# Kernel tuning notes

Measured on AMD Instinct MI355X. Metric: run time of the kernel, lower is better.

## Reference

```python
import jax, jax.numpy as jnp
import numpy as np

N_NODES = 20000
N_EDGES = 320000
IN_F = 168
HID = 256


def gcn_conv(x, W, b, src, dst, ew, n_nodes):
    """PyG GCNConv: symmetric normalization with self-loops (fill 1.0).
    out = D^-1/2 (A + I) D^-1/2 X W^T + b, aggregated at dst (source_to_target).
    """
    xw = x @ W.T  # [N, F_out]
    # degree at target nodes, including self-loop weight 1.0
    deg = jax.ops.segment_sum(ew, dst, num_segments=n_nodes) + 1.0
    dinv = jnp.where(deg > 0, jax.lax.rsqrt(deg), 0.0)
    norm = dinv[src] * ew * dinv[dst]  # [E]
    agg = jax.ops.segment_sum(norm[:, None] * xw[src], dst, num_segments=n_nodes)
    # self-loop contribution: norm_ii = dinv[i]^2
    out = agg + (dinv * dinv)[:, None] * xw
    return out + b


def setup_inputs() -> dict:
    key = jax.random.key(0)
    k = jax.random.split(key, 8)
    x = jax.random.normal(k[0], (N_NODES, IN_F), dtype=jnp.float32)
    edge_index = jax.random.randint(k[1], (2, N_EDGES), 0, N_NODES, dtype=jnp.int64)
    edge_weight = jax.random.uniform(k[2], (N_EDGES,), dtype=jnp.float32)
    # GCN layer weights (PyG Linear: y = x W^T), plus per-layer bias
    s1 = 1.0 / np.sqrt(IN_F)
    s2 = 1.0 / np.sqrt(HID)
    W1 = jax.random.uniform(k[3], (HID, IN_F), minval=-s1, maxval=s1, dtype=jnp.float32)
    b1 = jnp.zeros((HID,), dtype=jnp.float32)
    W2 = jax.random.uniform(k[4], (HID, HID), minval=-s2, maxval=s2, dtype=jnp.float32)
    b2 = jnp.zeros((HID,), dtype=jnp.float32)
    return {"x": x, "edge_index": edge_index, "edge_weight": edge_weight,
            "W1": W1, "b1": b1, "W2": W2, "b2": b2}


def reference(x, edge_index, edge_weight, W1, b1, W2, b2):
    src, dst = edge_index[0], edge_index[1]
    h = gcn_conv(x, W1, b1, src, dst, edge_weight, N_NODES)
    h = jax.nn.relu(h)
    h = gcn_conv(h, W2, b2, src, dst, edge_weight, N_NODES)
    h = jax.nn.relu(h)
    return h
```

## Files before the change

kernel.cpp:

```cpp
#include <hip/hip_runtime.h>

#define N_NODES 20000
#define N_EDGES 320000
#define IN_F    168
#define HID     256
#define K1P     192
#define XS      192
#define NF4     42

typedef __attribute__((ext_vector_type(8))) short bf16x8;
typedef __attribute__((ext_vector_type(4))) float f32x4;

__device__ __forceinline__ short f2bf(float f) {
    union { float f; unsigned u; } v; v.f = f;
    unsigned r = v.u + 0x7FFFu + ((v.u >> 16) & 1u);
    return (short)(r >> 16);
}
__device__ __forceinline__ float bf2f(short s) {
    union { unsigned u; float f; } v; v.u = ((unsigned)(unsigned short)s) << 16;
    return v.f;
}


__global__ void prep_all(const float* __restrict__ x, short* __restrict__ xb,
                         const float* __restrict__ W1, const float* __restrict__ W2,
                         short* __restrict__ w1b, short* __restrict__ w2b,
                         const int* __restrict__ ei, const float* __restrict__ ew,
                         float* __restrict__ deg, int* __restrict__ counts) {
    int b = blockIdx.x;
    int k = threadIdx.x;
    if (b < N_NODES) {
        if (k >= XS) return;
        float v = (k < IN_F) ? x[(size_t)b * IN_F + k] : 0.f;
        xb[(size_t)b * XS + k] = f2bf(v);
        return;
    }
    b -= N_NODES;
    if (b < 256) {
        if (k >= K1P) return;
        float v = (k < IN_F) ? W1[(size_t)b * IN_F + k] : 0.f;
        w1b[(size_t)b * K1P + k] = f2bf(v);
        return;
    }
    if (b < 512) {
        int r = b - 256;
        w2b[(size_t)r * HID + k] = f2bf(W2[(size_t)r * HID + k]);
        return;
    }
    int e = (b - 512) * 256 + k;
    if (e < N_EDGES) {
        int d = ei[N_EDGES + e];
        atomicAdd(&deg[d], ew[e]);
        atomicAdd(&counts[d], 1);
    }
}


__global__ __launch_bounds__(1024) void scan_part(const int* __restrict__ counts,
                                                  int* __restrict__ offs,
                                                  int* __restrict__ bsum,
                                                  float* __restrict__ deg, int n) {
    int tid  = threadIdx.x;
    int lane = tid & 63;
    int wv   = tid >> 6;
    int i = blockIdx.x * 1024 + tid;
    if (i < n) deg[i] = rsqrtf(deg[i] + 1.0f);
    __shared__ int wsum[16];
    int v = (i < n) ? counts[i] : 0;
    int incl = v;
    #pragma unroll
    for (int d = 1; d < 64; d <<= 1) {
        int t = __shfl_up(incl, d);
        if (lane >= d) incl += t;
    }
    if (lane == 63) wsum[wv] = incl;
    __syncthreads();
    if (wv == 0) {
        int w = (lane < 16) ? wsum[lane] : 0;
        int winc = w;
        #pragma unroll
        for (int d = 1; d < 16; d <<= 1) {
            int t = __shfl_up(winc, d);
            if (lane >= d) winc += t;
        }
        if (lane < 16) wsum[lane] = winc - w;
    }
    __syncthreads();
    if (i < n) offs[i] = wsum[wv] + incl - v;
    if (tid == 1023) bsum[blockIdx.x] = wsum[15] + incl;
}

__global__ __launch_bounds__(1024) void scan_add(const int* __restrict__ bsum,
                                                 int* __restrict__ offs, int n) {
    int i = blockIdx.x * 1024 + threadIdx.x;
    int add = 0;
    for (int b = 0; b < (int)blockIdx.x; ++b) add += bsum[b];
    if (i < n) offs[i] += add;
    if (i == n) offs[n] = add + bsum[blockIdx.x];
}

__global__ void scatter_edges(const int* __restrict__ ei, const float* __restrict__ ew,
                              const float* __restrict__ dinv, const int* __restrict__ offs,
                              int* __restrict__ cursor, int2* __restrict__ er) {
    int e = blockIdx.x * blockDim.x + threadIdx.x;
    if (e >= N_EDGES) return;
    int s = ei[e];
    int d = ei[N_EDGES + e];
    int pos = offs[d] + atomicAdd(&cursor[d], 1);
    float nm = dinv[s] * ew[e] * dinv[d];
    er[pos] = make_int2(s, __float_as_int(nm));
}


__global__ __launch_bounds__(256) void agg_x(const short* __restrict__ xb,
                                             const float* __restrict__ dinv,
                                             const int* __restrict__ offs,
                                             const int2* __restrict__ er,
                                             short* __restrict__ ax) {
    int wave = threadIdx.x >> 6;
    int lane = threadIdx.x & 63;
    int n = blockIdx.x * 4 + wave;
    bool act = lane < NF4;
    int lo4 = act ? lane * 4 : 0;
    float di = dinv[n];
    float sw = di * di;
    short4 sv = *(const short4*)(xb + (size_t)n * XS + lo4);
    float a0 = sw * bf2f(sv.x), a1 = sw * bf2f(sv.y);
    float a2 = sw * bf2f(sv.z), a3 = sw * bf2f(sv.w);

    int p0 = offs[n], p1 = offs[n + 1];
    int p = p0;
    for (; p + 8 <= p1; p += 8) {
        int2 e[8]; short4 r[8];
        #pragma unroll
        for (int j = 0; j < 8; ++j) e[j] = er[p + j];
        #pragma unroll
        for (int j = 0; j < 8; ++j) r[j] = *(const short4*)(xb + (size_t)e[j].x * XS + lo4);
        #pragma unroll
        for (int j = 0; j < 8; ++j) {
            float w = __int_as_float(e[j].y);
            a0 += w * bf2f(r[j].x); a1 += w * bf2f(r[j].y);
            a2 += w * bf2f(r[j].z); a3 += w * bf2f(r[j].w);
        }
    }
    for (; p + 4 <= p1; p += 4) {
        int2 e[4]; short4 r[4];
        #pragma unroll
        for (int j = 0; j < 4; ++j) e[j] = er[p + j];
        #pragma unroll
        for (int j = 0; j < 4; ++j) r[j] = *(const short4*)(xb + (size_t)e[j].x * XS + lo4);
        #pragma unroll
        for (int j = 0; j < 4; ++j) {
            float w = __int_as_float(e[j].y);
            a0 += w * bf2f(r[j].x); a1 += w * bf2f(r[j].y);
            a2 += w * bf2f(r[j].z); a3 += w * bf2f(r[j].w);
        }
    }
    for (; p < p1; ++p) {
        int2 e0 = er[p];
        float w0 = __int_as_float(e0.y);
        short4 r0 = *(const short4*)(xb + (size_t)e0.x * XS + lo4);
        a0 += w0 * bf2f(r0.x); a1 += w0 * bf2f(r0.y);
        a2 += w0 * bf2f(r0.z); a3 += w0 * bf2f(r0.w);
    }

    size_t base = (size_t)n * K1P + lane * 4;
    if (act) {
        *(short4*)&ax[base] = make_short4(f2bf(a0), f2bf(a1), f2bf(a2), f2bf(a3));
    } else if (lane < 48) {
        *(short4*)&ax[base] = make_short4(0, 0, 0, 0);
    }
}

__global__ __launch_bounds__(256) void agg_h(const short* __restrict__ h1h,
                                             const float* __restrict__ dinv,
                                             const int* __restrict__ offs,
                                             const int2* __restrict__ er,
                                             short* __restrict__ ah) {
    int wave = threadIdx.x >> 6;
    int lane = threadIdx.x & 63;
    int n = blockIdx.x * 4 + wave;
    int lo4 = lane * 4;
    float di = dinv[n];
    float sw = di * di;
    short4 sv = *(const short4*)(h1h + (size_t)n * HID + lo4);
    float a0 = sw * bf2f(sv.x), a1 = sw * bf2f(sv.y);
    float a2 = sw * bf2f(sv.z), a3 = sw * bf2f(sv.w);

    int p0 = offs[n], p1 = offs[n + 1];
    int p = p0;
    for (; p + 8 <= p1; p += 8) {
        int2 e[8]; short4 r[8];
        #pragma unroll
        for (int j = 0; j < 8; ++j) e[j] = er[p + j];
        #pragma unroll
        for (int j = 0; j < 8; ++j) r[j] = *(const short4*)(h1h + (size_t)e[j].x * HID + lo4);
        #pragma unroll
        for (int j = 0; j < 8; ++j) {
            float w = __int_as_float(e[j].y);
            a0 += w * bf2f(r[j].x); a1 += w * bf2f(r[j].y);
            a2 += w * bf2f(r[j].z); a3 += w * bf2f(r[j].w);
        }
    }
    for (; p + 4 <= p1; p += 4) {
        int2 e[4]; short4 r[4];
        #pragma unroll
        for (int j = 0; j < 4; ++j) e[j] = er[p + j];
        #pragma unroll
        for (int j = 0; j < 4; ++j) r[j] = *(const short4*)(h1h + (size_t)e[j].x * HID + lo4);
        #pragma unroll
        for (int j = 0; j < 4; ++j) {
            float w = __int_as_float(e[j].y);
            a0 += w * bf2f(r[j].x); a1 += w * bf2f(r[j].y);
            a2 += w * bf2f(r[j].z); a3 += w * bf2f(r[j].w);
        }
    }
    for (; p < p1; ++p) {
        int2 e0 = er[p];
        float w0 = __int_as_float(e0.y);
        short4 r0 = *(const short4*)(h1h + (size_t)e0.x * HID + lo4);
        a0 += w0 * bf2f(r0.x); a1 += w0 * bf2f(r0.y);
        a2 += w0 * bf2f(r0.z); a3 += w0 * bf2f(r0.w);
    }

    size_t base = (size_t)n * HID + lo4;
    *(short4*)&ah[base] = make_short4(f2bf(a0), f2bf(a1), f2bf(a2), f2bf(a3));
}


#define LDS_STRIDE 72

__global__ __launch_bounds__(256) void gemm_bf(const short* __restrict__ Ah,
                                               const short* __restrict__ Wh,
                                               const float* __restrict__ bias,
                                               float* __restrict__ Cf,
                                               short* __restrict__ Cbf,
                                               int M, int Ks, int nsteps, int mode) {
    __shared__ short sAh[64 * LDS_STRIDE];
    __shared__ short sWh[64 * LDS_STRIDE];

    const int idx   = blockIdx.x;
    const int group = idx >> 5;
    const int xcd   = idx & 7;
    const int slot  = (idx >> 3) & 3;
    const int mt    = group * 8 + xcd;
    const int mtiles = (M + 63) >> 6;
    if (mt >= mtiles) return;
    const int bm = mt * 64;
    const int bn = slot * 64;

    const int tid  = threadIdx.x;
    const int lane = tid & 63;
    const int wv   = tid >> 6;
    const int l16  = lane & 15;
    const int quad = lane >> 4;
    const int wm   = (wv & 1) * 32;
    const int wn   = (wv >> 1) * 32;

    const int srow = tid >> 2;
    const int sseg = (tid & 3) * 16;
    int arow = bm + srow; if (arow >= M) arow = M - 1;
    const short* gAh = Ah + (size_t)arow * Ks;
    const short* gWh = Wh + (size_t)(bn + srow) * Ks;
    const int lds_off = srow * LDS_STRIDE + sseg;

    f32x4 acc00 = {0,0,0,0}, acc01 = {0,0,0,0}, acc10 = {0,0,0,0}, acc11 = {0,0,0,0};

    int4 pah0 = *(const int4*)(gAh + sseg), pah1 = *(const int4*)(gAh + sseg + 8);
    int4 pwh0 = *(const int4*)(gWh + sseg), pwh1 = *(const int4*)(gWh + sseg + 8);

    for (int ks = 0; ks < nsteps; ++ks) {
        *(int4*)&sAh[lds_off] = pah0; *(int4*)&sAh[lds_off + 8] = pah1;
        *(int4*)&sWh[lds_off] = pwh0; *(int4*)&sWh[lds_off + 8] = pwh1;
        __syncthreads();
        if (ks + 1 < nsteps) {
            int o = (ks + 1) * 64 + sseg;
            pah0 = *(const int4*)(gAh + o); pah1 = *(const int4*)(gAh + o + 8);
            pwh0 = *(const int4*)(gWh + o); pwh1 = *(const int4*)(gWh + o + 8);
        }
        #pragma unroll
        for (int o = 0; o < 2; ++o) {
            const int a0 = (wm + l16) * LDS_STRIDE + o * 32 + quad * 8;
            const int a1 = a0 + 16 * LDS_STRIDE;
            const int w0 = (wn + l16) * LDS_STRIDE + o * 32 + quad * 8;
            const int w1 = w0 + 16 * LDS_STRIDE;
            bf16x8 ah0 = *(const bf16x8*)&sAh[a0];
            bf16x8 ah1 = *(const bf16x8*)&sAh[a1];
            bf16x8 wh0 = *(const bf16x8*)&sWh[w0];
            bf16x8 wh1 = *(const bf16x8*)&sWh[w1];
            acc00 = __builtin_amdgcn_mfma_f32_16x16x32_bf16(ah0, wh0, acc00, 0, 0, 0);
            acc01 = __builtin_amdgcn_mfma_f32_16x16x32_bf16(ah0, wh1, acc01, 0, 0, 0);
            acc10 = __builtin_amdgcn_mfma_f32_16x16x32_bf16(ah1, wh0, acc10, 0, 0, 0);
            acc11 = __builtin_amdgcn_mfma_f32_16x16x32_bf16(ah1, wh1, acc11, 0, 0, 0);
        }
        __syncthreads();
    }

    const int colb = bn + wn + l16;
    const int rowb = bm + wm + quad * 4;
    const float b0 = bias[colb];
    const float b1 = bias[colb + 16];
    #pragma unroll
    for (int r = 0; r < 4; ++r) {
        int row = rowb + r;
        if (row < M) {
            float v0 = acc00[r] + b0; v0 = v0 > 0.f ? v0 : 0.f;
            float v1 = acc01[r] + b1; v1 = v1 > 0.f ? v1 : 0.f;
            if (mode == 0) {
                Cbf[(size_t)row * HID + colb]      = f2bf(v0);
                Cbf[(size_t)row * HID + colb + 16] = f2bf(v1);
            } else {
                Cf[(size_t)row * HID + colb]      = v0;
                Cf[(size_t)row * HID + colb + 16] = v1;
            }
        }
        int row2 = row + 16;
        if (row2 < M) {
            float v0 = acc10[r] + b0; v0 = v0 > 0.f ? v0 : 0.f;
            float v1 = acc11[r] + b1; v1 = v1 > 0.f ? v1 : 0.f;
            if (mode == 0) {
                Cbf[(size_t)row2 * HID + colb]      = f2bf(v0);
                Cbf[(size_t)row2 * HID + colb + 16] = f2bf(v1);
            } else {
                Cf[(size_t)row2 * HID + colb]      = v0;
                Cf[(size_t)row2 * HID + colb + 16] = v1;
            }
        }
    }
}


extern "C" void kernel_launch(void* const* d_in, const int* in_sizes, int n_in,
                              void* d_out, int out_size, void* d_ws, size_t ws_size,
                              hipStream_t stream) {
    const float* x  = (const float*)d_in[0];
    const int*   ei = (const int*)d_in[1];
    const float* ew = (const float*)d_in[2];
    const float* W1 = (const float*)d_in[3];
    const float* b1 = (const float*)d_in[4];
    const float* W2 = (const float*)d_in[5];
    const float* b2 = (const float*)d_in[6];
    float* out = (float*)d_out;

    char* ws = (char*)d_ws;
    float* deg      = (float*)(ws);
    int*   counts   = (int*)(ws + 80000);
    int*   cursor   = (int*)(ws + 160000);
    int*   offs     = (int*)(ws + 240000);
    int*   bsum     = (int*)(ws + 320016);
    int2*  er       = (int2*)(ws + 320144);
    short* ax       = (short*)(ws + 2880144);
    short* ah       = (short*)(ws + 2880144);
    short* h1h      = (short*)(ws + 23360144);
    short* w1b      = (short*)(ws + 33600144);
    short* w2b      = (short*)(ws + 33698448);
    short* xb       = (short*)(ws + 34058896);

    hipMemsetAsync(d_ws, 0, 240000, stream);

    const int TB = 256;
    prep_all<<<N_NODES + 512 + (N_EDGES + 255) / 256, 256, 0, stream>>>(
        x, xb, W1, W2, w1b, w2b, ei, ew, deg, counts);
    scan_part<<<20, 1024, 0, stream>>>(counts, offs, bsum, deg, N_NODES);
    scan_add<<<20, 1024, 0, stream>>>(bsum, offs, N_NODES);
    scatter_edges<<<(N_EDGES + TB - 1) / TB, TB, 0, stream>>>(ei, ew, deg, offs, cursor, er);

    const int mtiles = (N_NODES + 63) / 64;
    const int gemm_grid = ((mtiles + 7) / 8) * 32;
    agg_x<<<N_NODES / 4, 256, 0, stream>>>(xb, deg, offs, er, ax);
    gemm_bf<<<gemm_grid, 256, 0, stream>>>(ax, w1b, b1, nullptr, h1h,
                                           N_NODES, K1P, 3, 0);
    agg_h<<<N_NODES / 4, 256, 0, stream>>>(h1h, deg, offs, er, ah);
    gemm_bf<<<gemm_grid, 256, 0, stream>>>(ah, w2b, b2, out, nullptr,
                                           N_NODES, HID, 4, 1);
}
```

Measured before the change: 200.4 us.

## Pad CSR rows to multiples of eight and vectorize gather and prep

Each node's CSR edge list is rounded up to a multiple of eight entries, and the padding is filled with zero-weight edges pointing at node 0. This lets the aggregation kernels use a single unrolled 8-wide loop with int4 edge loads and no tail loops. The aggregation arithmetic now uses packed float2 math on bf16 pairs, and the prep kernel converts four floats per thread instead of one. The cost is extra padded edges to read and gather (up to seven per node), plus a wider memset and a padding fill pass in scatter_edges.

New measurement: 200.1 us. About the same (-0.1%).

```diff
diff --git a/kernel.cpp b/kernel.cpp
--- a/kernel.cpp
+++ b/kernel.cpp
@@ -7,50 +7,73 @@
 #define K1P     192
 #define XS      192
 #define NF4     42
+#define X4      48
 
 typedef __attribute__((ext_vector_type(8))) short bf16x8;
 typedef __attribute__((ext_vector_type(4))) float f32x4;
+typedef __attribute__((ext_vector_type(2))) float f32x2;
 
 __device__ __forceinline__ short f2bf(float f) {
     union { float f; unsigned u; } v; v.f = f;
     unsigned r = v.u + 0x7FFFu + ((v.u >> 16) & 1u);
     return (short)(r >> 16);
 }
-__device__ __forceinline__ float bf2f(short s) {
-    union { unsigned u; float f; } v; v.u = ((unsigned)(unsigned short)s) << 16;
-    return v.f;
-}
-
+__device__ __forceinline__ f32x2 bfp(unsigned u) {
+    f32x2 r;
+    r.x = __uint_as_float(u << 16);
+    r.y = __uint_as_float(u & 0xFFFF0000u);
+    return r;
+}
 
 __global__ void prep_all(const float* __restrict__ x, short* __restrict__ xb,
                          const float* __restrict__ W1, const float* __restrict__ W2,
                          short* __restrict__ w1b, short* __restrict__ w2b,
                          const int* __restrict__ ei, const float* __restrict__ ew,
                          float* __restrict__ deg, int* __restrict__ counts) {
-    int b = blockIdx.x;
-    int k = threadIdx.x;
-    if (b < N_NODES) {
-        if (k >= XS) return;
-        float v = (k < IN_F) ? x[(size_t)b * IN_F + k] : 0.f;
-        xb[(size_t)b * XS + k] = f2bf(v);
+    const int xTot  = N_NODES * X4;
+    const int w1Tot = 256 * X4;
+    const int w2Tot = 256 * 64;
+    int i = blockIdx.x * 256 + threadIdx.x;
+    if (i < xTot) {
+        int n  = i / X4;
+        int k4 = i - n * X4;
+        short4 o;
+        if (k4 < NF4) {
+            float4 v = *(const float4*)(x + (size_t)n * IN_F + k4 * 4);
+            o = make_short4(f2bf(v.x), f2bf(v.y), f2bf(v.z), f2bf(v.w));
+        } else {
+            o = make_short4(0, 0, 0, 0);
+        }
+        *(short4*)(xb + (size_t)n * XS + k4 * 4) = o;
         return;
     }
-    b -= N_NODES;
-    if (b < 256) {
-        if (k >= K1P) return;
-        float v = (k < IN_F) ? W1[(size_t)b * IN_F + k] : 0.f;
-        w1b[(size_t)b * K1P + k] = f2bf(v);
+    i -= xTot;
+    if (i < w1Tot) {
+        int r  = i / X4;
+        int k4 = i - r * X4;
+        short4 o;
+        if (k4 < NF4) {
+            float4 v = *(const float4*)(W1 + (size_t)r * IN_F + k4 * 4);
+            o = make_short4(f2bf(v.x), f2bf(v.y), f2bf(v.z), f2bf(v.w));
+        } else {
+            o = make_short4(0, 0, 0, 0);
+        }
+        *(short4*)(w1b + (size_t)r * K1P + k4 * 4) = o;
         return;
     }
-    if (b < 512) {
-        int r = b - 256;
-        w2b[(size_t)r * HID + k] = f2bf(W2[(size_t)r * HID + k]);
+    i -= w1Tot;
+    if (i < w2Tot) {
+        int r  = i >> 6;
+        int c4 = i & 63;
+        float4 v = *(const float4*)(W2 + (size_t)r * HID + c4 * 4);
+        *(short4*)(w2b + (size_t)r * HID + c4 * 4) =
+            make_short4(f2bf(v.x), f2bf(v.y), f2bf(v.z), f2bf(v.w));
         return;
     }
-    int e = (b - 512) * 256 + k;
-    if (e < N_EDGES) {
-        int d = ei[N_EDGES + e];
-        atomicAdd(&deg[d], ew[e]);
+    i -= w2Tot;
+    if (i < N_EDGES) {
+        int d = ei[N_EDGES + i];
+        atomicAdd(&deg[d], ew[i]);
         atomicAdd(&counts[d], 1);
     }
 }
@@ -66,7 +89,7 @@
     int i = blockIdx.x * 1024 + tid;
     if (i < n) deg[i] = rsqrtf(deg[i] + 1.0f);
     __shared__ int wsum[16];
-    int v = (i < n) ? counts[i] : 0;
+    int v = (i < n) ? ((counts[i] + 7) & ~7) : 0;
     int incl = v;
     #pragma unroll
     for (int d = 1; d < 64; d <<= 1) {
@@ -101,14 +124,23 @@
 
 __global__ void scatter_edges(const int* __restrict__ ei, const float* __restrict__ ew,
                               const float* __restrict__ dinv, const int* __restrict__ offs,
+                              const int* __restrict__ counts,
                               int* __restrict__ cursor, int2* __restrict__ er) {
-    int e = blockIdx.x * blockDim.x + threadIdx.x;
-    if (e >= N_EDGES) return;
-    int s = ei[e];
-    int d = ei[N_EDGES + e];
-    int pos = offs[d] + atomicAdd(&cursor[d], 1);
-    float nm = dinv[s] * ew[e] * dinv[d];
-    er[pos] = make_int2(s, __float_as_int(nm));
+    int t = blockIdx.x * 256 + threadIdx.x;
+    if (t < N_EDGES) {
+        int s = ei[t];
+        int d = ei[N_EDGES + t];
+        int pos = offs[d] + atomicAdd(&cursor[d], 1);
+        float nm = dinv[s] * ew[t] * dinv[d];
+        er[pos] = make_int2(s, __float_as_int(nm));
+        return;
+    }
+    int n = t - N_EDGES;
+    if (n < N_NODES) {
+        int p   = offs[n] + counts[n];
+        int end = offs[n + 1];
+        for (; p < end; ++p) er[p] = make_int2(0, 0);
+    }
 }
 
 
@@ -124,49 +156,40 @@
     int lo4 = act ? lane * 4 : 0;
     float di = dinv[n];
     float sw = di * di;
-    short4 sv = *(const short4*)(xb + (size_t)n * XS + lo4);
-    float a0 = sw * bf2f(sv.x), a1 = sw * bf2f(sv.y);
-    float a2 = sw * bf2f(sv.z), a3 = sw * bf2f(sv.w);
+    uint2 sv = *(const uint2*)(xb + (size_t)n * XS + lo4);
+    f32x2 a01 = bfp(sv.x) * sw;
+    f32x2 a23 = bfp(sv.y) * sw;
 
     int p0 = offs[n], p1 = offs[n + 1];
-    int p = p0;
-    for (; p + 8 <= p1; p += 8) {
-        int2 e[8]; short4 r[8];
-        #pragma unroll
-        for (int j = 0; j < 8; ++j) e[j] = er[p + j];
-        #pragma unroll
-        for (int j = 0; j < 8; ++j) r[j] = *(const short4*)(xb + (size_t)e[j].x * XS + lo4);
-        #pragma unroll
-        for (int j = 0; j < 8; ++j) {
-            float w = __int_as_float(e[j].y);
-            a0 += w * bf2f(r[j].x); a1 += w * bf2f(r[j].y);
-            a2 += w * bf2f(r[j].z); a3 += w * bf2f(r[j].w);
-        }
-    }
-    for (; p + 4 <= p1; p += 4) {
-        int2 e[4]; short4 r[4];
-        #pragma unroll
-        for (int j = 0; j < 4; ++j) e[j] = er[p + j];
-        #pragma unroll
-        for (int j = 0; j < 4; ++j) r[j] = *(const short4*)(xb + (size_t)e[j].x * XS + lo4);
-        #pragma unroll
-        for (int j = 0; j < 4; ++j) {
-            float w = __int_as_float(e[j].y);
-            a0 += w * bf2f(r[j].x); a1 += w * bf2f(r[j].y);
-            a2 += w * bf2f(r[j].z); a3 += w * bf2f(r[j].w);
-        }
-    }
-    for (; p < p1; ++p) {
-        int2 e0 = er[p];
-        float w0 = __int_as_float(e0.y);
-        short4 r0 = *(const short4*)(xb + (size_t)e0.x * XS + lo4);
-        a0 += w0 * bf2f(r0.x); a1 += w0 * bf2f(r0.y);
-        a2 += w0 * bf2f(r0.z); a3 += w0 * bf2f(r0.w);
+    for (int p = p0; p < p1; p += 8) {
+        const int4* e4 = (const int4*)(er + p);
+        int4 eA = e4[0], eB = e4[1], eC = e4[2], eD = e4[3];
+        uint2 r0 = *(const uint2*)(xb + (size_t)eA.x * XS + lo4);
+        uint2 r1 = *(const uint2*)(xb + (size_t)eA.z * XS + lo4);
+        uint2 r2 = *(const uint2*)(xb + (size_t)eB.x * XS + lo4);
+        uint2 r3 = *(const uint2*)(xb + (size_t)eB.z * XS + lo4);
+        uint2 r4 = *(const uint2*)(xb + (size_t)eC.x * XS + lo4);
+        uint2 r5 = *(const uint2*)(xb + (size_t)eC.z * XS + lo4);
+        uint2 r6 = *(const uint2*)(xb + (size_t)eD.x * XS + lo4);
+        uint2 r7 = *(const uint2*)(xb + (size_t)eD.z * XS + lo4);
+        float w0 = __int_as_float(eA.y), w1 = __int_as_float(eA.w);
+        float w2 = __int_as_float(eB.y), w3 = __int_as_float(eB.w);
+        float w4 = __int_as_float(eC.y), w5 = __int_as_float(eC.w);
+        float w6 = __int_as_float(eD.y), w7 = __int_as_float(eD.w);
+        a01 += bfp(r0.x) * w0; a23 += bfp(r0.y) * w0;
+        a01 += bfp(r1.x) * w1; a23 += bfp(r1.y) * w1;
+        a01 += bfp(r2.x) * w2; a23 += bfp(r2.y) * w2;
+        a01 += bfp(r3.x) * w3; a23 += bfp(r3.y) * w3;
+        a01 += bfp(r4.x) * w4; a23 += bfp(r4.y) * w4;
+        a01 += bfp(r5.x) * w5; a23 += bfp(r5.y) * w5;
+        a01 += bfp(r6.x) * w6; a23 += bfp(r6.y) * w6;
+        a01 += bfp(r7.x) * w7; a23 += bfp(r7.y) * w7;
     }
 
     size_t base = (size_t)n * K1P + lane * 4;
     if (act) {
-        *(short4*)&ax[base] = make_short4(f2bf(a0), f2bf(a1), f2bf(a2), f2bf(a3));
+        *(short4*)&ax[base] = make_short4(f2bf(a01.x), f2bf(a01.y),
+                                          f2bf(a23.x), f2bf(a23.y));
     } else if (lane < 48) {
         *(short4*)&ax[base] = make_short4(0, 0, 0, 0);
     }
@@ -183,48 +206,38 @@
     int lo4 = lane * 4;
     float di = dinv[n];
     float sw = di * di;
-    short4 sv = *(const short4*)(h1h + (size_t)n * HID + lo4);
-    float a0 = sw * bf2f(sv.x), a1 = sw * bf2f(sv.y);
-    float a2 = sw * bf2f(sv.z), a3 = sw * bf2f(sv.w);
+    uint2 sv = *(const uint2*)(h1h + (size_t)n * HID + lo4);
+    f32x2 a01 = bfp(sv.x) * sw;
+    f32x2 a23 = bfp(sv.y) * sw;
 
     int p0 = offs[n], p1 = offs[n + 1];
-    int p = p0;
-    for (; p + 8 <= p1; p += 8) {
-        int2 e[8]; short4 r[8];
-        #pragma unroll
-        for (int j = 0; j < 8; ++j) e[j] = er[p + j];
-        #pragma unroll
-        for (int j = 0; j < 8; ++j) r[j] = *(const short4*)(h1h + (size_t)e[j].x * HID + lo4);
-        #pragma unroll
-        for (int j = 0; j < 8; ++j) {
-            float w = __int_as_float(e[j].y);
-            a0 += w * bf2f(r[j].x); a1 += w * bf2f(r[j].y);
-            a2 += w * bf2f(r[j].z); a3 += w * bf2f(r[j].w);
-        }
-    }
-    for (; p + 4 <= p1; p += 4) {
-        int2 e[4]; short4 r[4];
-        #pragma unroll
-        for (int j = 0; j < 4; ++j) e[j] = er[p + j];
-        #pragma unroll
-        for (int j = 0; j < 4; ++j) r[j] = *(const short4*)(h1h + (size_t)e[j].x * HID + lo4);
-        #pragma unroll
-        for (int j = 0; j < 4; ++j) {
-            float w = __int_as_float(e[j].y);
-            a0 += w * bf2f(r[j].x); a1 += w * bf2f(r[j].y);
-            a2 += w * bf2f(r[j].z); a3 += w * bf2f(r[j].w);
-        }
-    }
-    for (; p < p1; ++p) {
-        int2 e0 = er[p];
-        float w0 = __int_as_float(e0.y);
-        short4 r0 = *(const short4*)(h1h + (size_t)e0.x * HID + lo4);
-        a0 += w0 * bf2f(r0.x); a1 += w0 * bf2f(r0.y);
-        a2 += w0 * bf2f(r0.z); a3 += w0 * bf2f(r0.w);
-    }
-
-    size_t base = (size_t)n * HID + lo4;
-    *(short4*)&ah[base] = make_short4(f2bf(a0), f2bf(a1), f2bf(a2), f2bf(a3));
+    for (int p = p0; p < p1; p += 8) {
+        const int4* e4 = (const int4*)(er + p);
+        int4 eA = e4[0], eB = e4[1], eC = e4[2], eD = e4[3];
+        uint2 r0 = *(const uint2*)(h1h + (size_t)eA.x * HID + lo4);
+        uint2 r1 = *(const uint2*)(h1h + (size_t)eA.z * HID + lo4);
+        uint2 r2 = *(const uint2*)(h1h + (size_t)eB.x * HID + lo4);
+        uint2 r3 = *(const uint2*)(h1h + (size_t)eB.z * HID + lo4);
+        uint2 r4 = *(const uint2*)(h1h + (size_t)eC.x * HID + lo4);
+        uint2 r5 = *(const uint2*)(h1h + (size_t)eC.z * HID + lo4);
+        uint2 r6 = *(const uint2*)(h1h + (size_t)eD.x * HID + lo4);
+        uint2 r7 = *(const uint2*)(h1h + (size_t)eD.z * HID + lo4);
+        float w0 = __int_as_float(eA.y), w1 = __int_as_float(eA.w);
+        float w2 = __int_as_float(eB.y), w3 = __int_as_float(eB.w);
+        float w4 = __int_as_float(eC.y), w5 = __int_as_float(eC.w);
+        float w6 = __int_as_float(eD.y), w7 = __int_as_float(eD.w);
+        a01 += bfp(r0.x) * w0; a23 += bfp(r0.y) * w0;
+        a01 += bfp(r1.x) * w1; a23 += bfp(r1.y) * w1;
+        a01 += bfp(r2.x) * w2; a23 += bfp(r2.y) * w2;
+        a01 += bfp(r3.x) * w3; a23 += bfp(r3.y) * w3;
+        a01 += bfp(r4.x) * w4; a23 += bfp(r4.y) * w4;
+        a01 += bfp(r5.x) * w5; a23 += bfp(r5.y) * w5;
+        a01 += bfp(r6.x) * w6; a23 += bfp(r6.y) * w6;
+        a01 += bfp(r7.x) * w7; a23 += bfp(r7.y) * w7;
+    }
+
+    *(short4*)&ah[(size_t)n * HID + lo4] = make_short4(f2bf(a01.x), f2bf(a01.y),
+                                                       f2bf(a23.x), f2bf(a23.y));
 }
 
 
@@ -349,21 +362,22 @@
     int*   offs     = (int*)(ws + 240000);
     int*   bsum     = (int*)(ws + 320016);
     int2*  er       = (int2*)(ws + 320144);
-    short* ax       = (short*)(ws + 2880144);
-    short* ah       = (short*)(ws + 2880144);
-    short* h1h      = (short*)(ws + 23360144);
-    short* w1b      = (short*)(ws + 33600144);
-    short* w2b      = (short*)(ws + 33698448);
-    short* xb       = (short*)(ws + 34058896);
-
-    hipMemsetAsync(d_ws, 0, 240000, stream);
-
-    const int TB = 256;
-    prep_all<<<N_NODES + 512 + (N_EDGES + 255) / 256, 256, 0, stream>>>(
+    short* ax       = (short*)(ws + 4160144);
+    short* ah       = (short*)(ws + 4160144);
+    short* h1h      = (short*)(ws + 14400144);
+    short* w1b      = (short*)(ws + 24640144);
+    short* w2b      = (short*)(ws + 24738448);
+    short* xb       = (short*)(ws + 24869520);
+
+    hipMemsetAsync(d_ws, 0, 320144, stream);
+
+    const int prep_tot = N_NODES * X4 + 256 * X4 + 256 * 64 + N_EDGES;
+    prep_all<<<(prep_tot + 255) / 256, 256, 0, stream>>>(
         x, xb, W1, W2, w1b, w2b, ei, ew, deg, counts);
     scan_part<<<20, 1024, 0, stream>>>(counts, offs, bsum, deg, N_NODES);
     scan_add<<<20, 1024, 0, stream>>>(bsum, offs, N_NODES);
-    scatter_edges<<<(N_EDGES + TB - 1) / TB, TB, 0, stream>>>(ei, ew, deg, offs, cursor, er);
+    const int sc_blocks = (N_EDGES + N_NODES + 255) / 256;
+    scatter_edges<<<sc_blocks, 256, 0, stream>>>(ei, ew, deg, offs, counts, cursor, er);
 
     const int mtiles = (N_NODES + 63) / 64;
     const int gemm_grid = ((mtiles + 7) / 8) * 32;
```
